# Optimization experiments

Measured on AMD Instinct MI355X. Metric: run time of the kernel, lower is better.

Reference implementation:

```python
import jax, jax.numpy as jnp
import numpy as np

G = 64; B = 4; PER = 25000; N = B * PER
C_SEM = 64; C_MOS = 64; C = 32; NCLS = 26
OFFS = [(dx, dy, dz) for dx in (-1, 0, 1) for dy in (-1, 0, 1) for dz in (-1, 0, 1)]  # 27 kernel offsets


def _build_sparse():
    """Random active voxels per batch + [N,27] submanifold neighbor map (-1 = absent)."""
    rng = np.random.default_rng(0)
    keys_l, coords_l = [], []
    for b in range(B):
        lin = np.sort(rng.choice(G ** 3, size=PER, replace=False))
        x, y, z = lin // (G * G), (lin // G) % G, lin % G
        coords_l.append(np.stack([np.full(PER, b), x, y, z], 1))
        keys_l.append(b * (G ** 3) + lin)
    keys = np.concatenate(keys_l)
    co = np.concatenate(coords_l)
    order = np.argsort(keys, kind='stable')
    sk = keys[order]
    nbr = np.full((N, 27), -1, np.int64)
    bx, x, y, z = co[:, 0], co[:, 1], co[:, 2], co[:, 3]
    for k, (dx, dy, dz) in enumerate(OFFS):
        nx, ny, nz = x + dx, y + dy, z + dz
        ok = (nx >= 0) & (nx < G) & (ny >= 0) & (ny < G) & (nz >= 0) & (nz < G)
        nk = bx * (G ** 3) + nx * (G * G) + ny * G + nz
        pos = np.clip(np.searchsorted(sk, nk), 0, N - 1)
        hit = ok & (sk[pos] == nk)
        nbr[:, k] = np.where(hit, order[pos], -1)
    return co[:, 0].astype(np.int32), nbr.astype(np.int32)


def setup_inputs() -> dict:
    key = jax.random.key(0)
    ks = jax.random.split(key, 16)
    bids, nbr = _build_sparse()
    nrm = lambda k, s: jax.random.normal(ks[k], s, jnp.float32) * 0.05
    return {
        'feat_sem': jax.random.normal(ks[0], (N, C_SEM), jnp.float32),
        'feat_mos': jax.random.normal(ks[1], (N, C_MOS), jnp.float32),
        'fus_sp_w': nrm(2, (C_MOS, 1)), 'fus_sp_b': jnp.zeros((1,), jnp.float32),
        'fus_ch_w': nrm(3, (C_SEM, C_SEM)), 'fus_ch_b': jnp.zeros((C_SEM,), jnp.float32),
        'conv_w': nrm(4, (27, C_SEM, C)), 'conv_b': jnp.zeros((C,), jnp.float32),
        'r1c1_w': nrm(5, (27, C, C)), 'r1g1': jnp.ones((C,), jnp.float32), 'r1b1': jnp.zeros((C,), jnp.float32),
        'r1c2_w': nrm(6, (27, C, C)), 'r1g2': jnp.ones((C,), jnp.float32), 'r1b2': jnp.zeros((C,), jnp.float32),
        'ca1_w': nrm(7, (C, C // 8)), 'ca2_w': nrm(8, (C // 8, C)),
        'r2c1_w': nrm(9, (27, C, C)), 'r2g1': jnp.ones((C,), jnp.float32), 'r2b1': jnp.zeros((C,), jnp.float32),
        'r2c2_w': nrm(10, (27, C, C)), 'r2g2': jnp.ones((C,), jnp.float32), 'r2b2': jnp.zeros((C,), jnp.float32),
        'out_g': jnp.ones((C,), jnp.float32), 'out_b': jnp.zeros((C,), jnp.float32),
        'lin_w': nrm(11, (C, NCLS)), 'lin_b': jnp.zeros((NCLS,), jnp.float32),
        'batch_ids': jnp.asarray(bids), 'nbr': jnp.asarray(nbr), 'num_batches': B,
    }


def _subm3(x, W, nbr, b=None):
    # x: [N,Cin], W: [27,Cin,Cout], nbr: [N,27] (-1 = missing neighbor)
    valid = nbr >= 0
    g = x[jnp.where(valid, nbr, 0)] * valid[..., None].astype(x.dtype)  # [N,27,Cin]
    out = jnp.einsum('nkc,kco->no', g, W)
    return out if b is None else out + b


def _bn(x, g, b, eps=1e-4):
    # BatchNorm1d in training mode: batch stats over N, biased variance
    m = jnp.mean(x, 0)
    v = jnp.mean((x - m) ** 2, 0)
    return (x - m) * jax.lax.rsqrt(v + eps) * g + b


def _seg_mean(x, ids, nb):
    s = jax.ops.segment_sum(x, ids, num_segments=nb)
    c = jax.ops.segment_sum(jnp.ones((x.shape[0], 1), x.dtype), ids, num_segments=nb)
    return s / c


def _forward(feat_sem, feat_mos, fus_sp_w, fus_sp_b, fus_ch_w, fus_ch_b, conv_w, conv_b,
             r1c1_w, r1g1, r1b1, r1c2_w, r1g2, r1b2, ca1_w, ca2_w,
             r2c1_w, r2g1, r2b1, r2c2_w, r2g2, r2b2, out_g, out_b, lin_w, lin_b,
             batch_ids, nbr, num_batches):
    # ---- fusion_module_MGA_3D ----
    fm = jax.nn.sigmoid(feat_mos @ fus_sp_w + fus_sp_b) * feat_sem        # [N,Csem]
    vec = _seg_mean(fm, batch_ids, num_batches) @ fus_ch_w + fus_ch_b    # [B,Csem]
    vec = jax.nn.softmax(vec, axis=1) * vec.shape[1]
    fm = fm * vec[batch_ids]
    feat = fm + feat_sem
    # ---- conv ----
    h = _subm3(feat, conv_w, nbr, conv_b)                                # [N,32]

    def resblock(h, c1w, g1, b1, c2w, g2, b2):
        o = jax.nn.relu(_bn(_subm3(h, c1w, nbr), g1, b1))
        o = _bn(_subm3(o, c2w, nbr), g2, b2)
        return jax.nn.relu(o + h)

    h = resblock(h, r1c1_w, r1g1, r1b1, r1c2_w, r1g2, r1b2)
    # ---- ChannelAttention3D ----
    avg = _seg_mean(h, batch_ids, num_batches)
    mx = jax.ops.segment_max(h, batch_ids, num_segments=num_batches)
    mlp = lambda v: jax.nn.relu(v @ ca1_w) @ ca2_w
    att = jax.nn.sigmoid(mlp(avg) + mlp(mx))                             # [B,32]
    h = h * att[batch_ids]
    h = resblock(h, r2c1_w, r2g1, r2b1, r2c2_w, r2g2, r2b2)
    # ---- output layer ----
    h = jax.nn.relu(_bn(h, out_g, out_b))
    return h @ lin_w + lin_b                                             # [N,NCLS]


def reference(feat_sem, feat_mos, fus_sp_w, fus_sp_b, fus_ch_w, fus_ch_b, conv_w, conv_b,
              r1c1_w, r1g1, r1b1, r1c2_w, r1g2, r1b2, ca1_w, ca2_w,
              r2c1_w, r2g1, r2b1, r2c2_w, r2g2, r2b2, out_g, out_b, lin_w, lin_b,
              batch_ids, nbr, num_batches):
    return _forward(feat_sem, feat_mos, fus_sp_w, fus_sp_b, fus_ch_w, fus_ch_b, conv_w, conv_b,
                    r1c1_w, r1g1, r1b1, r1c2_w, r1g2, r1b2, ca1_w, ca2_w,
                    r2c1_w, r2g1, r2b1, r2c2_w, r2g2, r2b2, out_g, out_b, lin_w, lin_b,
                    batch_ids, nbr, num_batches)
```

## Files before the change

kernel.cpp:

```cpp
#include <hip/hip_runtime.h>
#include <math.h>

#define BMAX 4
typedef __attribute__((ext_vector_type(8))) short s16x8;
typedef __attribute__((ext_vector_type(4))) float f32x4;

__device__ __forceinline__ float sigmoidf_(float x) { return 1.f / (1.f + expf(-x)); }

__device__ __forceinline__ ushort f2b(float f) {
    uint u = __float_as_uint(f);
    u = u + 0x7FFFu + ((u >> 16) & 1u);
    return (ushort)(u >> 16);
}
__device__ __forceinline__ uint pk2(float a, float b) {
    return (uint)f2b(a) | ((uint)f2b(b) << 16);
}

__global__ __launch_bounds__(256)
void k_fuse_s(const float* __restrict__ mos, const float* __restrict__ spw,
              const float* __restrict__ spb, const int* __restrict__ bids,
              float* __restrict__ s_out, float* __restrict__ cnt, int N)
{
    __shared__ float lcnt[BMAX];
    int tid = threadIdx.x;
    if (tid < BMAX) lcnt[tid] = 0.f;
    __syncthreads();
    int n = blockIdx.x * 256 + tid;
    if (n < N) {
        const float* mr = mos + (size_t)n * 64;
        float dot = 0.f;
        #pragma unroll
        for (int c = 0; c < 64; c += 4) {
            float4 m4 = *(const float4*)(mr + c);
            float4 w4 = *(const float4*)(spw + c);
            dot += m4.x * w4.x + m4.y * w4.y + m4.z * w4.z + m4.w * w4.w;
        }
        float s = sigmoidf_(dot + spb[0]);
        s_out[n] = s;
        atomicAdd(&lcnt[bids[n]], 1.f);
    }
    __syncthreads();
    if (tid < BMAX && lcnt[tid] != 0.f) atomicAdd(&cnt[tid], lcnt[tid]);
}

__global__ __launch_bounds__(256)
void k_seg_part(const float* __restrict__ fsem, const float* __restrict__ s_buf,
                const int* __restrict__ bids, float* __restrict__ part, int N)
{
    __shared__ float lseg[BMAX * 64];
    int tid = threadIdx.x;
    lseg[tid] = 0.f;
    __syncthreads();
    int c = tid & 63;
    int slot = blockIdx.x * 4 + (tid >> 6);
    int nslots = gridDim.x * 4;
    int chunk = (N + nslots - 1) / nslots;
    int n0 = slot * chunk;
    int n1 = min(N, n0 + chunk);
    float acc = 0.f; int curb = -1;
    int n = n0;
    for (; n + 4 <= n1; n += 4) {
        int b0 = bids[n], b3 = bids[n + 3];
        float s0 = s_buf[n], s1 = s_buf[n + 1], s2 = s_buf[n + 2], s3 = s_buf[n + 3];
        float f0 = fsem[(size_t)n * 64 + c];
        float f1 = fsem[(size_t)(n + 1) * 64 + c];
        float f2 = fsem[(size_t)(n + 2) * 64 + c];
        float f3 = fsem[(size_t)(n + 3) * 64 + c];
        if (b0 == b3) {
            if (b0 != curb) {
                if (curb >= 0) atomicAdd(&lseg[curb * 64 + c], acc);
                acc = 0.f; curb = b0;
            }
            acc += s0 * f0 + s1 * f1 + s2 * f2 + s3 * f3;
        } else {
            int bb[4] = { b0, bids[n + 1], bids[n + 2], b3 };
            float sv[4] = { s0, s1, s2, s3 };
            float fv[4] = { f0, f1, f2, f3 };
            #pragma unroll
            for (int q = 0; q < 4; ++q) {
                if (bb[q] != curb) {
                    if (curb >= 0) atomicAdd(&lseg[curb * 64 + c], acc);
                    acc = 0.f; curb = bb[q];
                }
                acc += sv[q] * fv[q];
            }
        }
    }
    for (; n < n1; ++n) {
        int b = bids[n];
        if (b != curb) {
            if (curb >= 0) atomicAdd(&lseg[curb * 64 + c], acc);
            acc = 0.f; curb = b;
        }
        acc += s_buf[n] * fsem[(size_t)n * 64 + c];
    }
    if (curb >= 0) atomicAdd(&lseg[curb * 64 + c], acc);
    __syncthreads();
    part[(size_t)blockIdx.x * 256 + tid] = lseg[tid];
}

__global__ void k_seg_red(const float* __restrict__ part, float* __restrict__ seg, int nblk)
{
    int tid = threadIdx.x;
    float a = 0.f;
    #pragma unroll 8
    for (int i = 0; i < nblk; ++i) a += part[(size_t)i * 256 + tid];
    seg[tid] = a;
}

__global__ void k_vec(const float* __restrict__ seg, const float* __restrict__ cnt,
                      const float* __restrict__ chw, const float* __restrict__ chb,
                      float* __restrict__ vec)
{
    int b = threadIdx.x >> 6;
    int c = threadIdx.x & 63;
    float mean = seg[b * 64 + c] / cnt[b];
    float v = chb[c];
    #pragma unroll 1
    for (int i = 0; i < 64; ++i) {
        float mi = __shfl(mean, i, 64);
        v += mi * chw[i * 64 + c];
    }
    float m = v;
    #pragma unroll
    for (int off = 32; off; off >>= 1) m = fmaxf(m, __shfl_xor(m, off, 64));
    float e = expf(v - m);
    float ssum = e;
    #pragma unroll
    for (int off = 32; off; off >>= 1) ssum += __shfl_xor(ssum, off, 64);
    vec[b * 64 + c] = e / ssum * 64.f;
}

__global__ __launch_bounds__(256)
void k_gate_cvt(const float* __restrict__ fs, const float* __restrict__ s_buf,
                const float* __restrict__ vec, const int* __restrict__ bids,
                ushort* __restrict__ out, int N)
{
    int n = blockIdx.x * 256 + threadIdx.x;
    if (n >= N) return;
    float s = s_buf[n];
    const float* vr = vec + bids[n] * 64;
    const float* fr = fs + (size_t)n * 64;
    ushort* orow = out + (size_t)n * 64;
    #pragma unroll
    for (int c = 0; c < 64; c += 8) {
        float4 f0 = *(const float4*)(fr + c);
        float4 f1 = *(const float4*)(fr + c + 4);
        float4 v0 = *(const float4*)(vr + c);
        float4 v1 = *(const float4*)(vr + c + 4);
        float g0 = f0.x * (1.f + s * v0.x), g1 = f0.y * (1.f + s * v0.y);
        float g2 = f0.z * (1.f + s * v0.z), g3 = f0.w * (1.f + s * v0.w);
        float g4 = f1.x * (1.f + s * v1.x), g5 = f1.y * (1.f + s * v1.y);
        float g6 = f1.z * (1.f + s * v1.z), g7 = f1.w * (1.f + s * v1.w);
        uint4 o; o.x = pk2(g0, g1); o.y = pk2(g2, g3); o.z = pk2(g4, g5); o.w = pk2(g6, g7);
        *(uint4*)(orow + c) = o;
    }
}

__device__ __forceinline__ void wpack_one(const float* __restrict__ W, int CIN,
                                          int tt, ushort* __restrict__ dst)
{
    int nkc = CIN >> 5;
    int lane = tt & 63;
    int nt = (tt >> 6) & 1;
    int kc = (tt >> 7) % nkc;
    int k = tt / (nkc * 128);
    int kk = kc * 32 + (lane >> 4) * 8;
    int col = nt * 16 + (lane & 15);
    const float* src = W + ((size_t)k * CIN + kk) * 32 + col;
    float v[8];
    #pragma unroll
    for (int e = 0; e < 8; ++e) v[e] = src[e * 32];
    uint4 o; o.x = pk2(v[0], v[1]); o.y = pk2(v[2], v[3]);
    o.z = pk2(v[4], v[5]); o.w = pk2(v[6], v[7]);
    *(uint4*)(dst + (size_t)tt * 8) = o;
}

__global__ __launch_bounds__(256)
void k_wpack_all(const float* __restrict__ W0, const float* __restrict__ W1,
                 const float* __restrict__ W2, const float* __restrict__ W3,
                 const float* __restrict__ W4, ushort* __restrict__ P)
{
    int t = blockIdx.x * 256 + threadIdx.x;
    if (t < 6912) {
        wpack_one(W0, 64, t, P);
    } else {
        int r = t - 6912;
        int s = r / 3456;
        int tt = r % 3456;
        if (s >= 4) return;
        const float* W = (s == 0) ? W1 : (s == 1) ? W2 : (s == 2) ? W3 : W4;
        wpack_one(W, 32, tt, P + 55296 + s * 27648);
    }
}

template<int CIN, bool STATS, bool BIAS, bool WB16>
__global__ __launch_bounds__(256)
void k_mconv(const ushort* __restrict__ inb, const int* __restrict__ nbr,
             const ushort* __restrict__ wpk, const float* __restrict__ bias,
             float* __restrict__ outf, ushort* __restrict__ outb,
             float* __restrict__ bnsum, float* __restrict__ bnsq, int N)
{
    __shared__ float lsum[32];
    __shared__ float lsq[32];
    int tid = threadIdx.x;
    if (STATS) {
        if (tid < 32) { lsum[tid] = 0.f; lsq[tid] = 0.f; }
        __syncthreads();
    }
    int lane = tid & 63;
    int gw = (blockIdx.x * 256 + tid) >> 6;
    int vbase = gw * 32;
    bool wact = vbase < N;
    float ps0 = 0.f, pq0 = 0.f, ps1 = 0.f, pq1 = 0.f;
    if (wact) {
        int row = lane & 15;
        int koff = (lane >> 4) * 8;
        f32x4 acc00 = {0.f,0.f,0.f,0.f}, acc01 = {0.f,0.f,0.f,0.f};
        f32x4 acc10 = {0.f,0.f,0.f,0.f}, acc11 = {0.f,0.f,0.f,0.f};
        const int* nb0 = nbr + (size_t)(vbase + row) * 27;
        const int* nb1 = nbr + (size_t)(vbase + 16 + row) * 27;
        #pragma unroll
        for (int k = 0; k < 27; ++k) {
            int j0 = nb0[k];
            int j1 = nb1[k];
            #pragma unroll
            for (int kc = 0; kc < CIN / 32; ++kc) {
                s16x8 a0 = {0,0,0,0,0,0,0,0};
                s16x8 a1 = {0,0,0,0,0,0,0,0};
                if (j0 >= 0) a0 = *(const s16x8*)(inb + (size_t)j0 * CIN + kc * 32 + koff);
                if (j1 >= 0) a1 = *(const s16x8*)(inb + (size_t)j1 * CIN + kc * 32 + koff);
                const ushort* wb = wpk + (size_t)(k * (CIN / 32) + kc) * 1024 + lane * 8;
                s16x8 b0 = *(const s16x8*)(wb);
                s16x8 b1 = *(const s16x8*)(wb + 512);
                acc00 = __builtin_amdgcn_mfma_f32_16x16x32_bf16(a0, b0, acc00, 0, 0, 0);
                acc01 = __builtin_amdgcn_mfma_f32_16x16x32_bf16(a0, b1, acc01, 0, 0, 0);
                acc10 = __builtin_amdgcn_mfma_f32_16x16x32_bf16(a1, b0, acc10, 0, 0, 0);
                acc11 = __builtin_amdgcn_mfma_f32_16x16x32_bf16(a1, b1, acc11, 0, 0, 0);
            }
        }
        int ccol = lane & 15;
        int crow = (lane >> 4) * 4;
        float b0v = BIAS ? bias[ccol] : 0.f;
        float b1v = BIAS ? bias[16 + ccol] : 0.f;
        #pragma unroll
        for (int mt = 0; mt < 2; ++mt) {
            const f32x4& A0 = mt ? acc10 : acc00;
            const f32x4& A1 = mt ? acc11 : acc01;
            #pragma unroll
            for (int i = 0; i < 4; ++i) {
                int v = vbase + mt * 16 + crow + i;
                float x0 = A0[i] + b0v;
                float x1 = A1[i] + b1v;
                outf[(size_t)v * 32 + ccol] = x0;
                outf[(size_t)v * 32 + 16 + ccol] = x1;
                if (WB16) {
                    outb[(size_t)v * 32 + ccol] = f2b(x0);
                    outb[(size_t)v * 32 + 16 + ccol] = f2b(x1);
                }
                if (STATS) { ps0 += x0; pq0 += x0 * x0; ps1 += x1; pq1 += x1 * x1; }
            }
        }
    }
    if (STATS) {
        ps0 += __shfl_xor(ps0, 16, 64); ps0 += __shfl_xor(ps0, 32, 64);
        pq0 += __shfl_xor(pq0, 16, 64); pq0 += __shfl_xor(pq0, 32, 64);
        ps1 += __shfl_xor(ps1, 16, 64); ps1 += __shfl_xor(ps1, 32, 64);
        pq1 += __shfl_xor(pq1, 16, 64); pq1 += __shfl_xor(pq1, 32, 64);
        if (lane < 16) {
            atomicAdd(&lsum[lane], ps0);
            atomicAdd(&lsq[lane], pq0);
            atomicAdd(&lsum[16 + lane], ps1);
            atomicAdd(&lsq[16 + lane], pq1);
        }
        __syncthreads();
        if (tid < 32) { atomicAdd(&bnsum[tid], lsum[tid]); atomicAdd(&bnsq[tid], lsq[tid]); }
    }
}

__global__ void k_stats(const float* __restrict__ sum, const float* __restrict__ sq,
                        const float* __restrict__ g, const float* __restrict__ bb,
                        float* __restrict__ sc, float* __restrict__ sh, float invN)
{
    int c = threadIdx.x;
    if (c < 32) {
        float m = sum[c] * invN;
        float v = sq[c] * invN - m * m;
        float s = g[c] * rsqrtf(v + 1e-4f);
        sc[c] = s;
        sh[c] = bb[c] - m * s;
    }
}

__global__ __launch_bounds__(256)
void k_bnact(const float* __restrict__ t, const float* __restrict__ sc,
             const float* __restrict__ sh, ushort* __restrict__ out, int N)
{
    int n = blockIdx.x * 256 + threadIdx.x;
    if (n >= N) return;
    const float* tr = t + (size_t)n * 32;
    ushort* orow = out + (size_t)n * 32;
    #pragma unroll
    for (int c = 0; c < 32; c += 8) {
        float4 t0 = *(const float4*)(tr + c);
        float4 t1 = *(const float4*)(tr + c + 4);
        float g0 = fmaxf(t0.x * sc[c+0] + sh[c+0], 0.f);
        float g1 = fmaxf(t0.y * sc[c+1] + sh[c+1], 0.f);
        float g2 = fmaxf(t0.z * sc[c+2] + sh[c+2], 0.f);
        float g3 = fmaxf(t0.w * sc[c+3] + sh[c+3], 0.f);
        float g4 = fmaxf(t1.x * sc[c+4] + sh[c+4], 0.f);
        float g5 = fmaxf(t1.y * sc[c+5] + sh[c+5], 0.f);
        float g6 = fmaxf(t1.z * sc[c+6] + sh[c+6], 0.f);
        float g7 = fmaxf(t1.w * sc[c+7] + sh[c+7], 0.f);
        uint4 o; o.x = pk2(g0, g1); o.y = pk2(g2, g3); o.z = pk2(g4, g5); o.w = pk2(g6, g7);
        *(uint4*)(orow + c) = o;
    }
}

__global__ __launch_bounds__(256)
void k_comb1(const float* __restrict__ t, const float* __restrict__ res,
             const float* __restrict__ sc, const float* __restrict__ sh,
             const int* __restrict__ bids, float* __restrict__ hout,
             float* __restrict__ seg_sum, float* __restrict__ seg_max, int N)
{
    __shared__ float lsum[BMAX * 32];
    __shared__ int   lmax[BMAX * 32];
    int tid = threadIdx.x;
    if (tid < BMAX * 32) { lsum[tid] = 0.f; lmax[tid] = 0; }
    __syncthreads();
    int n = blockIdx.x * 256 + tid;
    if (n < N) {
        int b = bids[n];
        const float* tr = t + (size_t)n * 32;
        const float* rr = res + (size_t)n * 32;
        float vals[32];
        #pragma unroll
        for (int c = 0; c < 32; c += 4) {
            float4 tv = *(const float4*)(tr + c);
            float4 rv = *(const float4*)(rr + c);
            vals[c + 0] = fmaxf(tv.x * sc[c + 0] + sh[c + 0] + rv.x, 0.f);
            vals[c + 1] = fmaxf(tv.y * sc[c + 1] + sh[c + 1] + rv.y, 0.f);
            vals[c + 2] = fmaxf(tv.z * sc[c + 2] + sh[c + 2] + rv.z, 0.f);
            vals[c + 3] = fmaxf(tv.w * sc[c + 3] + sh[c + 3] + rv.w, 0.f);
            float4 ov; ov.x = vals[c+0]; ov.y = vals[c+1]; ov.z = vals[c+2]; ov.w = vals[c+3];
            *(float4*)(hout + (size_t)n * 32 + c) = ov;
        }
        #pragma unroll
        for (int i = 0; i < 32; ++i) {
            int c = (tid + i) & 31;
            atomicAdd(&lsum[b * 32 + c], vals[c]);
            atomicMax(&lmax[b * 32 + c], __float_as_int(vals[c]));
        }
    }
    __syncthreads();
    if (tid < BMAX * 32) {
        atomicAdd(&seg_sum[tid], lsum[tid]);
        atomicMax((int*)(seg_max + tid), lmax[tid]);
    }
}

__global__ void k_att(const float* __restrict__ seg_sum, const float* __restrict__ seg_max,
                      const float* __restrict__ cnt, const float* __restrict__ ca1,
                      const float* __restrict__ ca2, float* __restrict__ att)
{
    int b = threadIdx.x >> 6;
    int lane = threadIdx.x & 63;
    bool actc = lane < 32;
    int c = lane & 31;
    float avg = actc ? seg_sum[b * 32 + c] / cnt[b] : 0.f;
    float mx  = actc ? seg_max[b * 32 + c] : 0.f;
    float h[8];
    #pragma unroll
    for (int i = 0; i < 4; ++i) {
        float w = actc ? ca1[c * 4 + i] : 0.f;
        h[i] = avg * w;
        h[i + 4] = mx * w;
    }
    #pragma unroll
    for (int off = 32; off; off >>= 1) {
        #pragma unroll
        for (int i = 0; i < 8; ++i) h[i] += __shfl_xor(h[i], off, 64);
    }
    if (actc) {
        float o = 0.f;
        #pragma unroll
        for (int i = 0; i < 4; ++i)
            o += (fmaxf(h[i], 0.f) + fmaxf(h[i + 4], 0.f)) * ca2[i * 32 + c];
        att[b * 32 + c] = sigmoidf_(o);
    }
}

__global__ __launch_bounds__(256)
void k_scale_cvt(const float* __restrict__ h1, const float* __restrict__ att,
                 const int* __restrict__ bids, float* __restrict__ hatt,
                 ushort* __restrict__ hattb, int N)
{
    int n = blockIdx.x * 256 + threadIdx.x;
    if (n >= N) return;
    const float* hr = h1 + (size_t)n * 32;
    const float* ar = att + bids[n] * 32;
    float* of = hatt + (size_t)n * 32;
    ushort* ob = hattb + (size_t)n * 32;
    #pragma unroll
    for (int c = 0; c < 32; c += 8) {
        float4 h0 = *(const float4*)(hr + c);
        float4 h1v = *(const float4*)(hr + c + 4);
        float4 a0 = *(const float4*)(ar + c);
        float4 a1 = *(const float4*)(ar + c + 4);
        float g0 = h0.x * a0.x, g1 = h0.y * a0.y, g2 = h0.z * a0.z, g3 = h0.w * a0.w;
        float g4 = h1v.x * a1.x, g5 = h1v.y * a1.y, g6 = h1v.z * a1.z, g7 = h1v.w * a1.w;
        float4 w0; w0.x = g0; w0.y = g1; w0.z = g2; w0.w = g3;
        float4 w1; w1.x = g4; w1.y = g5; w1.z = g6; w1.w = g7;
        *(float4*)(of + c) = w0;
        *(float4*)(of + c + 4) = w1;
        uint4 o; o.x = pk2(g0, g1); o.y = pk2(g2, g3); o.z = pk2(g4, g5); o.w = pk2(g6, g7);
        *(uint4*)(ob + c) = o;
    }
}

__global__ __launch_bounds__(256)
void k_comb2(const float* __restrict__ t, const float* __restrict__ hres,
             const float* __restrict__ sc, const float* __restrict__ sh,
             float* __restrict__ hout, float* __restrict__ bnsum,
             float* __restrict__ bnsq, int N)
{
    __shared__ float lsum[32];
    __shared__ float lsq[32];
    int tid = threadIdx.x;
    if (tid < 32) { lsum[tid] = 0.f; lsq[tid] = 0.f; }
    __syncthreads();
    int n = blockIdx.x * 256 + tid;
    bool act = n < N;
    float vals[32];
    if (act) {
        const float* tr = t + (size_t)n * 32;
        const float* hr = hres + (size_t)n * 32;
        #pragma unroll
        for (int c = 0; c < 32; c += 4) {
            float4 tv = *(const float4*)(tr + c);
            float4 hv = *(const float4*)(hr + c);
            vals[c + 0] = fmaxf(tv.x * sc[c + 0] + sh[c + 0] + hv.x, 0.f);
            vals[c + 1] = fmaxf(tv.y * sc[c + 1] + sh[c + 1] + hv.y, 0.f);
            vals[c + 2] = fmaxf(tv.z * sc[c + 2] + sh[c + 2] + hv.z, 0.f);
            vals[c + 3] = fmaxf(tv.w * sc[c + 3] + sh[c + 3] + hv.w, 0.f);
            float4 ov; ov.x = vals[c+0]; ov.y = vals[c+1]; ov.z = vals[c+2]; ov.w = vals[c+3];
            *(float4*)(hout + (size_t)n * 32 + c) = ov;
        }
    } else {
        #pragma unroll
        for (int c = 0; c < 32; ++c) vals[c] = 0.f;
    }
    #pragma unroll
    for (int i = 0; i < 32; ++i) {
        int c = (tid + i) & 31;
        atomicAdd(&lsum[c], vals[c]);
        atomicAdd(&lsq[c], vals[c] * vals[c]);
    }
    __syncthreads();
    if (tid < 32) { atomicAdd(&bnsum[tid], lsum[tid]); atomicAdd(&bnsq[tid], lsq[tid]); }
}

__global__ __launch_bounds__(256)
void k_final(const float* __restrict__ h2, const float* __restrict__ sc,
             const float* __restrict__ sh, const float* __restrict__ lw,
             const float* __restrict__ lb, float* __restrict__ out, int N)
{
    int n = blockIdx.x * 256 + threadIdx.x;
    if (n >= N) return;
    const float* hr = h2 + (size_t)n * 32;
    float acc[26];
    #pragma unroll
    for (int o = 0; o < 26; ++o) acc[o] = lb[o];
    #pragma unroll
    for (int c4 = 0; c4 < 32; c4 += 4) {
        float4 hv = *(const float4*)(hr + c4);
        float xs[4] = { hv.x, hv.y, hv.z, hv.w };
        #pragma unroll
        for (int cc = 0; cc < 4; ++cc) {
            int c = c4 + cc;
            float x = fmaxf(xs[cc] * sc[c] + sh[c], 0.f);
            const float* wr = lw + c * 26;
            #pragma unroll
            for (int o = 0; o < 26; ++o) acc[o] += x * wr[o];
        }
    }
    float* orow = out + (size_t)n * 26;
    #pragma unroll
    for (int o = 0; o < 26; ++o) orow[o] = acc[o];
}

extern "C" void kernel_launch(void* const* d_in, const int* in_sizes, int n_in,
                              void* d_out, int out_size, void* d_ws, size_t ws_size,
                              hipStream_t stream)
{
    const float* feat_sem = (const float*)d_in[0];
    const float* feat_mos = (const float*)d_in[1];
    const float* fus_sp_w = (const float*)d_in[2];
    const float* fus_sp_b = (const float*)d_in[3];
    const float* fus_ch_w = (const float*)d_in[4];
    const float* fus_ch_b = (const float*)d_in[5];
    const float* conv_w   = (const float*)d_in[6];
    const float* conv_b   = (const float*)d_in[7];
    const float* r1c1_w   = (const float*)d_in[8];
    const float* r1g1     = (const float*)d_in[9];
    const float* r1b1     = (const float*)d_in[10];
    const float* r1c2_w   = (const float*)d_in[11];
    const float* r1g2     = (const float*)d_in[12];
    const float* r1b2     = (const float*)d_in[13];
    const float* ca1_w    = (const float*)d_in[14];
    const float* ca2_w    = (const float*)d_in[15];
    const float* r2c1_w   = (const float*)d_in[16];
    const float* r2g1     = (const float*)d_in[17];
    const float* r2b1     = (const float*)d_in[18];
    const float* r2c2_w   = (const float*)d_in[19];
    const float* r2g2     = (const float*)d_in[20];
    const float* r2b2     = (const float*)d_in[21];
    const float* out_g    = (const float*)d_in[22];
    const float* out_b    = (const float*)d_in[23];
    const float* lin_w    = (const float*)d_in[24];
    const float* lin_b    = (const float*)d_in[25];
    const int*   bids     = (const int*)d_in[26];
    const int*   nbr      = (const int*)d_in[27];
    int N = in_sizes[0] / 64;

    float* ws = (float*)d_ws;
    float* S1 = ws;
    float* S2 = ws + (size_t)32 * N;
    float* S3 = ws + (size_t)64 * N;
    float* S4 = ws + (size_t)96 * N;
    ushort* BB1 = (ushort*)(ws + (size_t)128 * N);
    ushort* BB2 = (ushort*)(ws + (size_t)144 * N);
    float* sbuf = (float*)BB2;
    ushort* FGB = (ushort*)S3;
    float* segpart = S2;
    float* st = ws + (size_t)160 * N;
    float* seg_fm = st;
    float* cnt    = st + 256;
    float* vec    = st + 260;
    float* bnsum  = st + 516;
    float* bnsq   = st + 676;
    float* bnsc   = st + 836;
    float* bnsh   = st + 996;
    float* seg1s  = st + 1156;
    float* seg1m  = st + 1284;
    float* att    = st + 1412;
    ushort* wpk0 = (ushort*)(st + 1600);
    ushort* wpk1 = wpk0 + 55296;
    ushort* wpk2 = wpk1 + 27648;
    ushort* wpk3 = wpk2 + 27648;
    ushort* wpk4 = wpk3 + 27648;

    hipMemsetAsync(st, 0, 1540 * sizeof(float), stream);

    int nb = (N + 255) / 256;
    int nw = (N + 127) / 128;
    const int NSEG = 512;
    float invN = 1.f / (float)N;

    k_wpack_all<<<81, 256, 0, stream>>>(conv_w, r1c1_w, r1c2_w, r2c1_w, r2c2_w, wpk0);

    k_fuse_s<<<nb, 256, 0, stream>>>(feat_mos, fus_sp_w, fus_sp_b, bids, sbuf, cnt, N);
    k_seg_part<<<NSEG, 256, 0, stream>>>(feat_sem, sbuf, bids, segpart, N);
    k_seg_red<<<1, 256, 0, stream>>>(segpart, seg_fm, NSEG);
    k_vec<<<1, 256, 0, stream>>>(seg_fm, cnt, fus_ch_w, fus_ch_b, vec);
    k_gate_cvt<<<nb, 256, 0, stream>>>(feat_sem, sbuf, vec, bids, FGB, N);

    k_mconv<64, false, true, true><<<nw, 256, 0, stream>>>(FGB, nbr, wpk0, conv_b,
        S1, BB1, nullptr, nullptr, N);

    k_mconv<32, true, false, false><<<nw, 256, 0, stream>>>(BB1, nbr, wpk1, nullptr,
        S2, nullptr, bnsum + 0, bnsq + 0, N);
    k_stats<<<1, 32, 0, stream>>>(bnsum + 0, bnsq + 0, r1g1, r1b1, bnsc + 0, bnsh + 0, invN);
    k_bnact<<<nb, 256, 0, stream>>>(S2, bnsc + 0, bnsh + 0, BB2, N);

    k_mconv<32, true, false, false><<<nw, 256, 0, stream>>>(BB2, nbr, wpk2, nullptr,
        S3, nullptr, bnsum + 32, bnsq + 32, N);
    k_stats<<<1, 32, 0, stream>>>(bnsum + 32, bnsq + 32, r1g2, r1b2, bnsc + 32, bnsh + 32, invN);

    k_comb1<<<nb, 256, 0, stream>>>(S3, S1, bnsc + 32, bnsh + 32, bids, S4, seg1s, seg1m, N);
    k_att<<<1, 256, 0, stream>>>(seg1s, seg1m, cnt, ca1_w, ca2_w, att);
    k_scale_cvt<<<nb, 256, 0, stream>>>(S4, att, bids, S2, BB1, N);

    k_mconv<32, true, false, false><<<nw, 256, 0, stream>>>(BB1, nbr, wpk3, nullptr,
        S1, nullptr, bnsum + 64, bnsq + 64, N);
    k_stats<<<1, 32, 0, stream>>>(bnsum + 64, bnsq + 64, r2g1, r2b1, bnsc + 64, bnsh + 64, invN);
    k_bnact<<<nb, 256, 0, stream>>>(S1, bnsc + 64, bnsh + 64, BB2, N);

    k_mconv<32, true, false, false><<<nw, 256, 0, stream>>>(BB2, nbr, wpk4, nullptr,
        S3, nullptr, bnsum + 96, bnsq + 96, N);
    k_stats<<<1, 32, 0, stream>>>(bnsum + 96, bnsq + 96, r2g2, r2b2, bnsc + 96, bnsh + 96, invN);

    k_comb2<<<nb, 256, 0, stream>>>(S3, S2, bnsc + 96, bnsh + 96, S4,
        bnsum + 128, bnsq + 128, N);
    k_stats<<<1, 32, 0, stream>>>(bnsum + 128, bnsq + 128, out_g, out_b, bnsc + 128, bnsh + 128, invN);

    k_final<<<nb, 256, 0, stream>>>(S4, bnsc + 128, bnsh + 128, lin_w, lin_b, (float*)d_out, N);
}
```

Before: 567.7 us.

## Replace global atomic reductions with per-block partials and tree reduction kernels

Global atomicAdd/atomicMax accumulation of BN statistics, batch counts and attention segment sums is replaced by per-block partial buffers reduced in dedicated reduction kernels (k_statsr, k_attred, wider k_seg_red). The memset is removed. comb1/comb2 now use four threads per voxel with 8 channels each, which raises parallelism and shortens each thread's chain of shared-memory atomics. The intent is to remove atomic contention on a few global addresses and the serial per-thread loops, at the cost of extra small launches and partial-buffer traffic.

```diff
diff --git a/kernel.cpp b/kernel.cpp
--- a/kernel.cpp
+++ b/kernel.cpp
@@ -19,7 +19,7 @@
 __global__ __launch_bounds__(256)
 void k_fuse_s(const float* __restrict__ mos, const float* __restrict__ spw,
               const float* __restrict__ spb, const int* __restrict__ bids,
-              float* __restrict__ s_out, float* __restrict__ cnt, int N)
+              float* __restrict__ s_out, float* __restrict__ pc, int N)
 {
     __shared__ float lcnt[BMAX];
     int tid = threadIdx.x;
@@ -40,7 +40,7 @@
         atomicAdd(&lcnt[bids[n]], 1.f);
     }
     __syncthreads();
-    if (tid < BMAX && lcnt[tid] != 0.f) atomicAdd(&cnt[tid], lcnt[tid]);
+    if (tid < BMAX) pc[(size_t)blockIdx.x * 4 + tid] = lcnt[tid];
 }
 
 __global__ __launch_bounds__(256)
@@ -99,22 +99,42 @@
     part[(size_t)blockIdx.x * 256 + tid] = lseg[tid];
 }
 
-__global__ void k_seg_red(const float* __restrict__ part, float* __restrict__ seg, int nblk)
-{
-    int tid = threadIdx.x;
+__global__ __launch_bounds__(1024)
+void k_seg_red(const float* __restrict__ part, float* __restrict__ seg, int nblk)
+{
+    __shared__ float l[1024];
+    int tid = threadIdx.x;
+    int col = tid & 255, grp = tid >> 8;
     float a = 0.f;
     #pragma unroll 8
-    for (int i = 0; i < nblk; ++i) a += part[(size_t)i * 256 + tid];
-    seg[tid] = a;
-}
-
-__global__ void k_vec(const float* __restrict__ seg, const float* __restrict__ cnt,
+    for (int j = grp; j < nblk; j += 4) a += part[(size_t)j * 256 + col];
+    l[tid] = a;
+    __syncthreads();
+    if (tid < 256) seg[tid] = l[tid] + l[256 + tid] + l[512 + tid] + l[768 + tid];
+}
+
+__global__ void k_vec(const float* __restrict__ seg, const float* __restrict__ pc, int nbc,
                       const float* __restrict__ chw, const float* __restrict__ chb,
-                      float* __restrict__ vec)
-{
-    int b = threadIdx.x >> 6;
-    int c = threadIdx.x & 63;
-    float mean = seg[b * 64 + c] / cnt[b];
+                      float* __restrict__ vec, float* __restrict__ cnt_out)
+{
+    __shared__ float lred[256];
+    __shared__ float lcnt[4];
+    int tid = threadIdx.x;
+    float a = 0.f;
+    for (int j = tid >> 2; j < nbc; j += 64) a += pc[(size_t)j * 4 + (tid & 3)];
+    lred[tid] = a;
+    __syncthreads();
+    if (tid < 4) {
+        float s = 0.f;
+        #pragma unroll 8
+        for (int j = 0; j < 64; ++j) s += lred[j * 4 + tid];
+        lcnt[tid] = s;
+        cnt_out[tid] = s;
+    }
+    __syncthreads();
+    int b = tid >> 6;
+    int c = tid & 63;
+    float mean = seg[b * 64 + c] / lcnt[b];
     float v = chb[c];
     #pragma unroll 1
     for (int i = 0; i < 64; ++i) {
@@ -199,7 +219,7 @@
 void k_mconv(const ushort* __restrict__ inb, const int* __restrict__ nbr,
              const ushort* __restrict__ wpk, const float* __restrict__ bias,
              float* __restrict__ outf, ushort* __restrict__ outb,
-             float* __restrict__ bnsum, float* __restrict__ bnsq, int N)
+             float* __restrict__ pp, int N)
 {
     __shared__ float lsum[32];
     __shared__ float lsq[32];
@@ -274,21 +294,39 @@
             atomicAdd(&lsq[16 + lane], pq1);
         }
         __syncthreads();
-        if (tid < 32) { atomicAdd(&bnsum[tid], lsum[tid]); atomicAdd(&bnsq[tid], lsq[tid]); }
-    }
-}
-
-__global__ void k_stats(const float* __restrict__ sum, const float* __restrict__ sq,
-                        const float* __restrict__ g, const float* __restrict__ bb,
-                        float* __restrict__ sc, float* __restrict__ sh, float invN)
-{
-    int c = threadIdx.x;
-    if (c < 32) {
-        float m = sum[c] * invN;
-        float v = sq[c] * invN - m * m;
-        float s = g[c] * rsqrtf(v + 1e-4f);
-        sc[c] = s;
-        sh[c] = bb[c] - m * s;
+        if (tid < 32) {
+            pp[(size_t)blockIdx.x * 64 + tid] = lsum[tid];
+            pp[(size_t)blockIdx.x * 64 + 32 + tid] = lsq[tid];
+        }
+    }
+}
+
+__global__ __launch_bounds__(1024)
+void k_statsr(const float* __restrict__ part, int nblk,
+              const float* __restrict__ g, const float* __restrict__ bb,
+              float* __restrict__ sc, float* __restrict__ sh, float invN)
+{
+    __shared__ float l[1024];
+    int tid = threadIdx.x;
+    int col = tid & 63, grp = tid >> 6;
+    float a = 0.f;
+    #pragma unroll 8
+    for (int j = grp; j < nblk; j += 16) a += part[(size_t)j * 64 + col];
+    l[tid] = a;
+    __syncthreads();
+    if (tid < 64) {
+        float s = 0.f;
+        #pragma unroll
+        for (int gq = 0; gq < 16; ++gq) s += l[gq * 64 + tid];
+        l[tid] = s;
+    }
+    __syncthreads();
+    if (tid < 32) {
+        float m = l[tid] * invN;
+        float v = l[32 + tid] * invN - m * m;
+        float s = g[tid] * rsqrtf(v + 1e-4f);
+        sc[tid] = s;
+        sh[tid] = bb[tid] - m * s;
     }
 }
 
@@ -321,54 +359,89 @@
 void k_comb1(const float* __restrict__ t, const float* __restrict__ res,
              const float* __restrict__ sc, const float* __restrict__ sh,
              const int* __restrict__ bids, float* __restrict__ hout,
-             float* __restrict__ seg_sum, float* __restrict__ seg_max, int N)
+             float* __restrict__ part, int N)
 {
     __shared__ float lsum[BMAX * 32];
     __shared__ int   lmax[BMAX * 32];
     int tid = threadIdx.x;
     if (tid < BMAX * 32) { lsum[tid] = 0.f; lmax[tid] = 0; }
     __syncthreads();
-    int n = blockIdx.x * 256 + tid;
+    int gid = blockIdx.x * 256 + tid;
+    int n = gid >> 2;
+    int c0 = (gid & 3) * 8;
     if (n < N) {
         int b = bids[n];
-        const float* tr = t + (size_t)n * 32;
-        const float* rr = res + (size_t)n * 32;
-        float vals[32];
-        #pragma unroll
-        for (int c = 0; c < 32; c += 4) {
-            float4 tv = *(const float4*)(tr + c);
-            float4 rv = *(const float4*)(rr + c);
-            vals[c + 0] = fmaxf(tv.x * sc[c + 0] + sh[c + 0] + rv.x, 0.f);
-            vals[c + 1] = fmaxf(tv.y * sc[c + 1] + sh[c + 1] + rv.y, 0.f);
-            vals[c + 2] = fmaxf(tv.z * sc[c + 2] + sh[c + 2] + rv.z, 0.f);
-            vals[c + 3] = fmaxf(tv.w * sc[c + 3] + sh[c + 3] + rv.w, 0.f);
-            float4 ov; ov.x = vals[c+0]; ov.y = vals[c+1]; ov.z = vals[c+2]; ov.w = vals[c+3];
-            *(float4*)(hout + (size_t)n * 32 + c) = ov;
-        }
-        #pragma unroll
-        for (int i = 0; i < 32; ++i) {
-            int c = (tid + i) & 31;
-            atomicAdd(&lsum[b * 32 + c], vals[c]);
-            atomicMax(&lmax[b * 32 + c], __float_as_int(vals[c]));
-        }
-    }
-    __syncthreads();
-    if (tid < BMAX * 32) {
-        atomicAdd(&seg_sum[tid], lsum[tid]);
-        atomicMax((int*)(seg_max + tid), lmax[tid]);
-    }
-}
-
-__global__ void k_att(const float* __restrict__ seg_sum, const float* __restrict__ seg_max,
-                      const float* __restrict__ cnt, const float* __restrict__ ca1,
-                      const float* __restrict__ ca2, float* __restrict__ att)
-{
-    int b = threadIdx.x >> 6;
-    int lane = threadIdx.x & 63;
+        const float* tr = t + (size_t)n * 32 + c0;
+        const float* rr = res + (size_t)n * 32 + c0;
+        float4 t0 = *(const float4*)tr, t1 = *(const float4*)(tr + 4);
+        float4 r0 = *(const float4*)rr, r1 = *(const float4*)(rr + 4);
+        float v[8];
+        v[0] = fmaxf(t0.x * sc[c0+0] + sh[c0+0] + r0.x, 0.f);
+        v[1] = fmaxf(t0.y * sc[c0+1] + sh[c0+1] + r0.y, 0.f);
+        v[2] = fmaxf(t0.z * sc[c0+2] + sh[c0+2] + r0.z, 0.f);
+        v[3] = fmaxf(t0.w * sc[c0+3] + sh[c0+3] + r0.w, 0.f);
+        v[4] = fmaxf(t1.x * sc[c0+4] + sh[c0+4] + r1.x, 0.f);
+        v[5] = fmaxf(t1.y * sc[c0+5] + sh[c0+5] + r1.y, 0.f);
+        v[6] = fmaxf(t1.z * sc[c0+6] + sh[c0+6] + r1.z, 0.f);
+        v[7] = fmaxf(t1.w * sc[c0+7] + sh[c0+7] + r1.w, 0.f);
+        float4 o0 = { v[0], v[1], v[2], v[3] };
+        float4 o1 = { v[4], v[5], v[6], v[7] };
+        *(float4*)(hout + (size_t)n * 32 + c0) = o0;
+        *(float4*)(hout + (size_t)n * 32 + c0 + 4) = o1;
+        int base = b * 32 + c0;
+        #pragma unroll
+        for (int i = 0; i < 8; ++i) {
+            atomicAdd(&lsum[base + i], v[i]);
+            atomicMax(&lmax[base + i], __float_as_int(v[i]));
+        }
+    }
+    __syncthreads();
+    if (tid < 128) part[(size_t)blockIdx.x * 256 + tid] = lsum[tid];
+    else           part[(size_t)blockIdx.x * 256 + tid] = __int_as_float(lmax[tid - 128]);
+}
+
+__global__ __launch_bounds__(256)
+void k_attred(const float* __restrict__ part, int nblk, float* __restrict__ out)
+{
+    int tid = threadIdx.x;
+    int blk = blockIdx.x;
+    if (tid < 128) {
+        float a = 0.f;
+        #pragma unroll 4
+        for (int j = blk; j < nblk; j += 64) a += part[(size_t)j * 256 + tid];
+        out[(size_t)blk * 256 + tid] = a;
+    } else {
+        float m = 0.f;
+        #pragma unroll 4
+        for (int j = blk; j < nblk; j += 64) m = fmaxf(m, part[(size_t)j * 256 + tid]);
+        out[(size_t)blk * 256 + tid] = m;
+    }
+}
+
+__global__ void k_att(const float* __restrict__ part2, const float* __restrict__ cnt,
+                      const float* __restrict__ ca1, const float* __restrict__ ca2,
+                      float* __restrict__ att)
+{
+    __shared__ float seg[256];
+    int tid = threadIdx.x;
+    if (tid < 128) {
+        float a = 0.f;
+        #pragma unroll 8
+        for (int j = 0; j < 64; ++j) a += part2[j * 256 + tid];
+        seg[tid] = a;
+    } else {
+        float m = 0.f;
+        #pragma unroll 8
+        for (int j = 0; j < 64; ++j) m = fmaxf(m, part2[j * 256 + tid]);
+        seg[tid] = m;
+    }
+    __syncthreads();
+    int b = tid >> 6;
+    int lane = tid & 63;
     bool actc = lane < 32;
     int c = lane & 31;
-    float avg = actc ? seg_sum[b * 32 + c] / cnt[b] : 0.f;
-    float mx  = actc ? seg_max[b * 32 + c] : 0.f;
+    float avg = actc ? seg[b * 32 + c] / cnt[b] : 0.f;
+    float mx  = actc ? seg[128 + b * 32 + c] : 0.f;
     float h[8];
     #pragma unroll
     for (int i = 0; i < 4; ++i) {
@@ -421,43 +494,45 @@
 __global__ __launch_bounds__(256)
 void k_comb2(const float* __restrict__ t, const float* __restrict__ hres,
              const float* __restrict__ sc, const float* __restrict__ sh,
-             float* __restrict__ hout, float* __restrict__ bnsum,
-             float* __restrict__ bnsq, int N)
+             float* __restrict__ hout, float* __restrict__ part, int N)
 {
     __shared__ float lsum[32];
     __shared__ float lsq[32];
     int tid = threadIdx.x;
     if (tid < 32) { lsum[tid] = 0.f; lsq[tid] = 0.f; }
     __syncthreads();
-    int n = blockIdx.x * 256 + tid;
-    bool act = n < N;
-    float vals[32];
-    if (act) {
-        const float* tr = t + (size_t)n * 32;
-        const float* hr = hres + (size_t)n * 32;
-        #pragma unroll
-        for (int c = 0; c < 32; c += 4) {
-            float4 tv = *(const float4*)(tr + c);
-            float4 hv = *(const float4*)(hr + c);
-            vals[c + 0] = fmaxf(tv.x * sc[c + 0] + sh[c + 0] + hv.x, 0.f);
-            vals[c + 1] = fmaxf(tv.y * sc[c + 1] + sh[c + 1] + hv.y, 0.f);
-            vals[c + 2] = fmaxf(tv.z * sc[c + 2] + sh[c + 2] + hv.z, 0.f);
-            vals[c + 3] = fmaxf(tv.w * sc[c + 3] + sh[c + 3] + hv.w, 0.f);
-            float4 ov; ov.x = vals[c+0]; ov.y = vals[c+1]; ov.z = vals[c+2]; ov.w = vals[c+3];
-            *(float4*)(hout + (size_t)n * 32 + c) = ov;
-        }
-    } else {
-        #pragma unroll
-        for (int c = 0; c < 32; ++c) vals[c] = 0.f;
-    }
-    #pragma unroll
-    for (int i = 0; i < 32; ++i) {
-        int c = (tid + i) & 31;
-        atomicAdd(&lsum[c], vals[c]);
-        atomicAdd(&lsq[c], vals[c] * vals[c]);
-    }
-    __syncthreads();
-    if (tid < 32) { atomicAdd(&bnsum[tid], lsum[tid]); atomicAdd(&bnsq[tid], lsq[tid]); }
+    int gid = blockIdx.x * 256 + tid;
+    int n = gid >> 2;
+    int c0 = (gid & 3) * 8;
+    if (n < N) {
+        const float* tr = t + (size_t)n * 32 + c0;
+        const float* hr = hres + (size_t)n * 32 + c0;
+        float4 t0 = *(const float4*)tr, t1 = *(const float4*)(tr + 4);
+        float4 h0 = *(const float4*)hr, h1 = *(const float4*)(hr + 4);
+        float v[8];
+        v[0] = fmaxf(t0.x * sc[c0+0] + sh[c0+0] + h0.x, 0.f);
+        v[1] = fmaxf(t0.y * sc[c0+1] + sh[c0+1] + h0.y, 0.f);
+        v[2] = fmaxf(t0.z * sc[c0+2] + sh[c0+2] + h0.z, 0.f);
+        v[3] = fmaxf(t0.w * sc[c0+3] + sh[c0+3] + h0.w, 0.f);
+        v[4] = fmaxf(t1.x * sc[c0+4] + sh[c0+4] + h1.x, 0.f);
+        v[5] = fmaxf(t1.y * sc[c0+5] + sh[c0+5] + h1.y, 0.f);
+        v[6] = fmaxf(t1.z * sc[c0+6] + sh[c0+6] + h1.z, 0.f);
+        v[7] = fmaxf(t1.w * sc[c0+7] + sh[c0+7] + h1.w, 0.f);
+        float4 o0 = { v[0], v[1], v[2], v[3] };
+        float4 o1 = { v[4], v[5], v[6], v[7] };
+        *(float4*)(hout + (size_t)n * 32 + c0) = o0;
+        *(float4*)(hout + (size_t)n * 32 + c0 + 4) = o1;
+        #pragma unroll
+        for (int i = 0; i < 8; ++i) {
+            atomicAdd(&lsum[c0 + i], v[i]);
+            atomicAdd(&lsq[c0 + i], v[i] * v[i]);
+        }
+    }
+    __syncthreads();
+    if (tid < 32) {
+        part[(size_t)blockIdx.x * 64 + tid] = lsum[tid];
+        part[(size_t)blockIdx.x * 64 + 32 + tid] = lsq[tid];
+    }
 }
 
 __global__ __launch_bounds__(256)
@@ -537,62 +612,59 @@
     float* seg_fm = st;
     float* cnt    = st + 256;
     float* vec    = st + 260;
-    float* bnsum  = st + 516;
-    float* bnsq   = st + 676;
-    float* bnsc   = st + 836;
-    float* bnsh   = st + 996;
-    float* seg1s  = st + 1156;
-    float* seg1m  = st + 1284;
-    float* att    = st + 1412;
-    ushort* wpk0 = (ushort*)(st + 1600);
+    float* bnsc   = st + 516;
+    float* bnsh   = st + 676;
+    float* attbuf = st + 840;
+    float* pcnt   = st + 2048;
+    float* at2    = st + 4096;
+    ushort* wpk0 = (ushort*)(st + 20480);
     ushort* wpk1 = wpk0 + 55296;
     ushort* wpk2 = wpk1 + 27648;
     ushort* wpk3 = wpk2 + 27648;
     ushort* wpk4 = wpk3 + 27648;
 
-    hipMemsetAsync(st, 0, 1540 * sizeof(float), stream);
-
-    int nb = (N + 255) / 256;
-    int nw = (N + 127) / 128;
+    int nb  = (N + 255) / 256;
+    int nw  = (N + 127) / 128;
+    int nb4 = (N + 63) / 64;
     const int NSEG = 512;
     float invN = 1.f / (float)N;
 
     k_wpack_all<<<81, 256, 0, stream>>>(conv_w, r1c1_w, r1c2_w, r2c1_w, r2c2_w, wpk0);
 
-    k_fuse_s<<<nb, 256, 0, stream>>>(feat_mos, fus_sp_w, fus_sp_b, bids, sbuf, cnt, N);
+    k_fuse_s<<<nb, 256, 0, stream>>>(feat_mos, fus_sp_w, fus_sp_b, bids, sbuf, pcnt, N);
     k_seg_part<<<NSEG, 256, 0, stream>>>(feat_sem, sbuf, bids, segpart, N);
-    k_seg_red<<<1, 256, 0, stream>>>(segpart, seg_fm, NSEG);
-    k_vec<<<1, 256, 0, stream>>>(seg_fm, cnt, fus_ch_w, fus_ch_b, vec);
+    k_seg_red<<<1, 1024, 0, stream>>>(segpart, seg_fm, NSEG);
+    k_vec<<<1, 256, 0, stream>>>(seg_fm, pcnt, nb, fus_ch_w, fus_ch_b, vec, cnt);
     k_gate_cvt<<<nb, 256, 0, stream>>>(feat_sem, sbuf, vec, bids, FGB, N);
 
     k_mconv<64, false, true, true><<<nw, 256, 0, stream>>>(FGB, nbr, wpk0, conv_b,
-        S1, BB1, nullptr, nullptr, N);
+        S1, BB1, nullptr, N);
 
     k_mconv<32, true, false, false><<<nw, 256, 0, stream>>>(BB1, nbr, wpk1, nullptr,
-        S2, nullptr, bnsum + 0, bnsq + 0, N);
-    k_stats<<<1, 32, 0, stream>>>(bnsum + 0, bnsq + 0, r1g1, r1b1, bnsc + 0, bnsh + 0, invN);
+        S2, nullptr, S4, N);
+    k_statsr<<<1, 1024, 0, stream>>>(S4, nw, r1g1, r1b1, bnsc + 0, bnsh + 0, invN);
     k_bnact<<<nb, 256, 0, stream>>>(S2, bnsc + 0, bnsh + 0, BB2, N);
 
     k_mconv<32, true, false, false><<<nw, 256, 0, stream>>>(BB2, nbr, wpk2, nullptr,
-        S3, nullptr, bnsum + 32, bnsq + 32, N);
-    k_stats<<<1, 32, 0, stream>>>(bnsum + 32, bnsq + 32, r1g2, r1b2, bnsc + 32, bnsh + 32, invN);
-
-    k_comb1<<<nb, 256, 0, stream>>>(S3, S1, bnsc + 32, bnsh + 32, bids, S4, seg1s, seg1m, N);
-    k_att<<<1, 256, 0, stream>>>(seg1s, seg1m, cnt, ca1_w, ca2_w, att);
-    k_scale_cvt<<<nb, 256, 0, stream>>>(S4, att, bids, S2, BB1, N);
+        S3, nullptr, S4, N);
+    k_statsr<<<1, 1024, 0, stream>>>(S4, nw, r1g2, r1b2, bnsc + 32, bnsh + 32, invN);
+
+    k_comb1<<<nb4, 256, 0, stream>>>(S3, S1, bnsc + 32, bnsh + 32, bids, S4, S2, N);
+    k_attred<<<64, 256, 0, stream>>>(S2, nb4, at2);
+    k_att<<<1, 256, 0, stream>>>(at2, cnt, ca1_w, ca2_w, attbuf);
+    k_scale_cvt<<<nb, 256, 0, stream>>>(S4, attbuf, bids, S2, BB1, N);
 
     k_mconv<32, true, false, false><<<nw, 256, 0, stream>>>(BB1, nbr, wpk3, nullptr,
-        S1, nullptr, bnsum + 64, bnsq + 64, N);
-    k_stats<<<1, 32, 0, stream>>>(bnsum + 64, bnsq + 64, r2g1, r2b1, bnsc + 64, bnsh + 64, invN);
+        S1, nullptr, S3, N);
+    k_statsr<<<1, 1024, 0, stream>>>(S3, nw, r2g1, r2b1, bnsc + 64, bnsh + 64, invN);
     k_bnact<<<nb, 256, 0, stream>>>(S1, bnsc + 64, bnsh + 64, BB2, N);
 
     k_mconv<32, true, false, false><<<nw, 256, 0, stream>>>(BB2, nbr, wpk4, nullptr,
-        S3, nullptr, bnsum + 96, bnsq + 96, N);
-    k_stats<<<1, 32, 0, stream>>>(bnsum + 96, bnsq + 96, r2g2, r2b2, bnsc + 96, bnsh + 96, invN);
-
-    k_comb2<<<nb, 256, 0, stream>>>(S3, S2, bnsc + 96, bnsh + 96, S4,
-        bnsum + 128, bnsq + 128, N);
-    k_stats<<<1, 32, 0, stream>>>(bnsum + 128, bnsq + 128, out_g, out_b, bnsc + 128, bnsh + 128, invN);
-
-    k_final<<<nb, 256, 0, stream>>>(S4, bnsc + 128, bnsh + 128, lin_w, lin_b, (float*)d_out, N);
-}
+        S3, nullptr, S4, N);
+    k_statsr<<<1, 1024, 0, stream>>>(S4, nw, r2g2, r2b2, bnsc + 96, bnsh + 96, invN);
+
+    k_comb2<<<nb4, 256, 0, stream>>>(S3, S2, bnsc + 96, bnsh + 96, S1, S4, N);
+    k_statsr<<<1, 1024, 0, stream>>>(S4, nb4, out_g, out_b, bnsc + 128, bnsh + 128, invN);
+
+    k_final<<<nb, 256, 0, stream>>>(S1, bnsc + 128, bnsh + 128, lin_w, lin_b, (float*)d_out, N);
+}
```

After: 515.7 us. -9.2%, faster.
